# Performance work log

Hardware: AMD Instinct MI355X
Metric: run time of the kernel (lower is better)

The kernel has to match this reference:

```python
import jax, jax.numpy as jnp
import numpy as np
import math

N_HEADS = 16
D_EMBED = 1024
D_HEAD = D_EMBED // N_HEADS


def setup_inputs() -> dict:
    key = jax.random.key(0)
    ks = jax.random.split(key, 5)
    B, T = 4, 2048
    x = jax.random.normal(ks[0], (B, T, D_EMBED), dtype=jnp.float32)
    s_in = 1.0 / math.sqrt(D_EMBED)
    W_in = jax.random.normal(ks[1], (3 * D_EMBED, D_EMBED), dtype=jnp.float32) * s_in
    b_in = jax.random.normal(ks[2], (3 * D_EMBED,), dtype=jnp.float32) * s_in
    W_out = jax.random.normal(ks[3], (D_EMBED, D_EMBED), dtype=jnp.float32) * s_in
    b_out = jax.random.normal(ks[4], (D_EMBED,), dtype=jnp.float32) * s_in
    return {"x": x, "W_in": W_in, "b_in": b_in, "W_out": W_out, "b_out": b_out,
            "causal_mask": 1}


def reference(x, W_in, b_in, W_out, b_out, causal_mask):
    B, T, C = x.shape
    # in_proj: x @ W_in^T + b_in -> (B,T,3C), chunk into q,k,v
    qkv = jnp.einsum('btc,ec->bte', x, W_in) + b_in
    q, k, v = jnp.split(qkv, 3, axis=-1)
    # (B,T,H,Dh) -> (B,H,T,Dh)
    def heads(t):
        return t.reshape(B, T, N_HEADS, D_HEAD).transpose(0, 2, 1, 3)
    q, k, v = heads(q), heads(k), heads(v)
    scores = jnp.einsum('bhqd,bhkd->bhqk', q, k) / math.sqrt(D_HEAD)
    if causal_mask:
        mask = jnp.triu(jnp.ones((T, T), dtype=bool), k=1)  # True above diagonal
        scores = jnp.where(mask, -jnp.inf, scores)
    attn = jax.nn.softmax(scores, axis=-1)
    out = jnp.einsum('bhqk,bhkd->bhqd', attn, v)
    out = out.transpose(0, 2, 1, 3).reshape(B, T, C)
    out = jnp.einsum('btc,oc->bto', out, W_out) + b_out
    return out
```

## Files before the change

kernel.cpp:

```cpp
#include <hip/hip_runtime.h>
#include <hip/hip_bf16.h>

#define T_SEQ 2048
#define D_EMB 1024
#define NH    16
#define DH    64
#define NB    4
#define MROWS (NB * T_SEQ)
#define QKVN  (3 * D_EMB)

typedef __attribute__((ext_vector_type(8))) short bf16x8;
typedef __attribute__((ext_vector_type(4))) float f32x4;

__device__ __forceinline__ unsigned short f2bf(float f) {
  __hip_bfloat16 h = __float2bfloat16(f);
  return __builtin_bit_cast(unsigned short, h);
}

__device__ __forceinline__ void gload_lds16(const void* g, void* lds) {
  __builtin_amdgcn_global_load_lds(
      (const __attribute__((address_space(1))) void*)g,
      (__attribute__((address_space(3))) void*)lds, 16, 0, 0);
}

__device__ __forceinline__ float redmax16(float v) {
  v = fmaxf(v, __shfl_xor(v, 1));
  v = fmaxf(v, __shfl_xor(v, 2));
  v = fmaxf(v, __shfl_xor(v, 4));
  v = fmaxf(v, __shfl_xor(v, 8));
  return v;
}
__device__ __forceinline__ float redsum16(float v) {
  v += __shfl_xor(v, 1);
  v += __shfl_xor(v, 2);
  v += __shfl_xor(v, 4);
  v += __shfl_xor(v, 8);
  return v;
}

__global__ __launch_bounds__(256) void cvt_kernel(const float* __restrict__ in,
                                                  unsigned short* __restrict__ out,
                                                  int n4) {
  for (int i = blockIdx.x * 256 + threadIdx.x; i < n4; i += gridDim.x * 256) {
    const float4 v = reinterpret_cast<const float4*>(in)[i];
    ushort4 o;
    o.x = f2bf(v.x); o.y = f2bf(v.y); o.z = f2bf(v.z); o.w = f2bf(v.w);
    reinterpret_cast<ushort4*>(out)[i] = o;
  }
}

template <int OUT_BF16>
__global__ __launch_bounds__(256) void gemm_bt(const unsigned short* __restrict__ A,
                                               const unsigned short* __restrict__ Bt,
                                               const float* __restrict__ bias,
                                               void* __restrict__ Cout,
                                               int M, int N, int K) {
  __shared__ __align__(16) unsigned short As[128 * 32];
  __shared__ __align__(16) unsigned short Bs[128 * 32];

  const int tid = threadIdx.x;
  const int w  = tid >> 6;
  const int l  = tid & 63;
  const int lr = l & 15;
  const int lk = (l >> 4) * 8;
  const int bm = blockIdx.y * 128;
  const int bn = blockIdx.x * 128;
  const int wr = (w >> 1) * 64;
  const int wc = (w & 1) * 64;

  f32x4 acc[4][4];
#pragma unroll
  for (int i = 0; i < 4; ++i)
#pragma unroll
    for (int j = 0; j < 4; ++j) acc[i][j] = (f32x4){0.f, 0.f, 0.f, 0.f};

  const int srow = l >> 2;
  const int sk   = (l & 3) * 8;
  const unsigned short* Ab = A + (size_t)(bm + w * 32 + srow) * K + sk;
  const unsigned short* Bb = Bt + (size_t)(bn + w * 32 + srow) * K + sk;

  for (int kt = 0; kt < K; kt += 32) {
    gload_lds16(Ab + kt,                  &As[(w * 32 + 0) * 32]);
    gload_lds16(Ab + kt + (size_t)16 * K, &As[(w * 32 + 16) * 32]);
    gload_lds16(Bb + kt,                  &Bs[(w * 32 + 0) * 32]);
    gload_lds16(Bb + kt + (size_t)16 * K, &Bs[(w * 32 + 16) * 32]);
    __syncthreads();

    bf16x8 a[4], b[4];
#pragma unroll
    for (int mi = 0; mi < 4; ++mi)
      a[mi] = *reinterpret_cast<const bf16x8*>(&As[(wr + mi * 16 + lr) * 32 + lk]);
#pragma unroll
    for (int ni = 0; ni < 4; ++ni)
      b[ni] = *reinterpret_cast<const bf16x8*>(&Bs[(wc + ni * 16 + lr) * 32 + lk]);
#pragma unroll
    for (int mi = 0; mi < 4; ++mi)
#pragma unroll
      for (int ni = 0; ni < 4; ++ni)
        acc[mi][ni] = __builtin_amdgcn_mfma_f32_16x16x32_bf16(a[mi], b[ni], acc[mi][ni], 0, 0, 0);
    __syncthreads();
  }

  const int lg = l >> 4;
#pragma unroll
  for (int mi = 0; mi < 4; ++mi)
#pragma unroll
    for (int ni = 0; ni < 4; ++ni)
#pragma unroll
      for (int i = 0; i < 4; ++i) {
        const int row = bm + wr + mi * 16 + lg * 4 + i;
        const int col = bn + wc + ni * 16 + lr;
        const float v = acc[mi][ni][i] + bias[col];
        if (OUT_BF16)
          ((unsigned short*)Cout)[(size_t)row * N + col] = f2bf(v);
        else
          ((float*)Cout)[(size_t)row * N + col] = v;
      }
}

__global__ __launch_bounds__(256) void attn_fwd(const unsigned short* __restrict__ qkv,
                                                unsigned short* __restrict__ attn_out,
                                                const int* __restrict__ causal_flag) {
  __shared__ __align__(16) unsigned short Ks[64 * 64];
  __shared__ __align__(16) unsigned short Vt[64 * 64];
  __shared__ __align__(16) unsigned short Ps[4][32 * 64];

  const int tid = threadIdx.x;
  const int w  = tid >> 6;
  const int l  = tid & 63;
  const int lr = l & 15;
  const int lg = l >> 4;
  const int lk = lg * 8;
  const int bx = blockIdx.x;
  const int bh = blockIdx.y;
  const int b  = bh >> 4;
  const int h  = bh & 15;
  const int causal = causal_flag[0];

  const unsigned short* Qp = qkv + (size_t)(b * T_SEQ) * QKVN + h * DH;
  const unsigned short* Kp = Qp + D_EMB;
  const unsigned short* Vp = Qp + 2 * D_EMB;

  for (int qq = 0; qq < 2; ++qq) {
    const int qt = qq ? (15 - bx) : bx;
    const int qbase = qt * 128;

    bf16x8 qf[2][2];
#pragma unroll
    for (int mi = 0; mi < 2; ++mi)
#pragma unroll
      for (int ks = 0; ks < 2; ++ks)
        qf[mi][ks] = *reinterpret_cast<const bf16x8*>(
            Qp + (size_t)(qbase + w * 32 + mi * 16 + lr) * QKVN + ks * 32 + lk);

    f32x4 oacc[2][4];
    float mrow[2][4], lsum[2][4];
#pragma unroll
    for (int mi = 0; mi < 2; ++mi) {
#pragma unroll
      for (int di = 0; di < 4; ++di) oacc[mi][di] = (f32x4){0.f, 0.f, 0.f, 0.f};
#pragma unroll
      for (int i = 0; i < 4; ++i) { mrow[mi][i] = -INFINITY; lsum[mi][i] = 0.f; }
    }

    const int nt = causal ? (qt * 2 + 2) : (T_SEQ / 64);

    for (int kb = 0; kb < nt; ++kb) {
      const int kbase = kb * 64;
#pragma unroll
      for (int i = 0; i < 2; ++i) {
        const int rloc = w * 16 + i * 8 + (l >> 3);
        const int cj   = (l & 7) ^ (l >> 3);
        gload_lds16(Kp + (size_t)(kbase + rloc) * QKVN + cj * 8,
                    &Ks[(w * 16 + i * 8) * 64]);
      }
#pragma unroll
      for (int g2 = 0; g2 < 2; ++g2) {
        const int idx = tid + g2 * 256;
        const int k   = idx & 63;
        const int d0  = (idx >> 6) * 8;
        bf16x8 v = *reinterpret_cast<const bf16x8*>(Vp + (size_t)(kbase + k) * QKVN + d0);
#pragma unroll
        for (int j = 0; j < 8; ++j)
          Vt[(d0 + j) * 64 + (k ^ (j << 3))] = ((unsigned short*)&v)[j];
      }
      __syncthreads();

      f32x4 s[2][4];
#pragma unroll
      for (int mi = 0; mi < 2; ++mi)
#pragma unroll
        for (int ni = 0; ni < 4; ++ni) s[mi][ni] = (f32x4){0.f, 0.f, 0.f, 0.f};
#pragma unroll
      for (int ks = 0; ks < 2; ++ks) {
        bf16x8 kf[4];
#pragma unroll
        for (int ni = 0; ni < 4; ++ni) {
          const int R = ni * 16 + lr;
          kf[ni] = *reinterpret_cast<const bf16x8*>(
              &Ks[R * 64 + (((ks * 4 + lg) ^ (R & 7)) << 3)]);
        }
#pragma unroll
        for (int mi = 0; mi < 2; ++mi)
#pragma unroll
          for (int ni = 0; ni < 4; ++ni)
            s[mi][ni] = __builtin_amdgcn_mfma_f32_16x16x32_bf16(qf[mi][ks], kf[ni], s[mi][ni], 0, 0, 0);
      }

      const bool mm = causal && (kbase + 64 > qbase);
#pragma unroll
      for (int mi = 0; mi < 2; ++mi) {
#pragma unroll
        for (int i = 0; i < 4; ++i) {
          const int qrow = qbase + w * 32 + mi * 16 + lg * 4 + i;
          float rmax = -INFINITY;
#pragma unroll
          for (int ni = 0; ni < 4; ++ni) {
            float v = s[mi][ni][i] * 0.125f;
            if (mm && (kbase + ni * 16 + lr > qrow)) v = -INFINITY;
            s[mi][ni][i] = v;
            rmax = fmaxf(rmax, v);
          }
          rmax = redmax16(rmax);
          const float mnew = fmaxf(mrow[mi][i], rmax);
          const float alpha = __expf(mrow[mi][i] - mnew);
          mrow[mi][i] = mnew;
          float psum = 0.f;
#pragma unroll
          for (int ni = 0; ni < 4; ++ni) {
            const float p = __expf(s[mi][ni][i] - mnew);
            s[mi][ni][i] = p;
            psum += p;
          }
          psum = redsum16(psum);
          lsum[mi][i] = lsum[mi][i] * alpha + psum;
#pragma unroll
          for (int di = 0; di < 4; ++di) oacc[mi][di][i] *= alpha;
          const int rp = mi * 16 + lg * 4 + i;
#pragma unroll
          for (int ni = 0; ni < 4; ++ni)
            Ps[w][rp * 64 + ((ni * 16 + lr) ^ ((rp & 7) << 3))] = f2bf(s[mi][ni][i]);
        }
      }
      __syncthreads();

#pragma unroll
      for (int ks2 = 0; ks2 < 2; ++ks2) {
        bf16x8 pf[2], vf[4];
#pragma unroll
        for (int mi = 0; mi < 2; ++mi) {
          const int R = mi * 16 + lr;
          pf[mi] = *reinterpret_cast<const bf16x8*>(
              &Ps[w][R * 64 + (((ks2 * 4 + lg) ^ (R & 7)) << 3)]);
        }
#pragma unroll
        for (int di = 0; di < 4; ++di) {
          const int R = di * 16 + lr;
          vf[di] = *reinterpret_cast<const bf16x8*>(
              &Vt[R * 64 + (((ks2 * 4 + lg) ^ (R & 7)) << 3)]);
        }
#pragma unroll
        for (int mi = 0; mi < 2; ++mi)
#pragma unroll
          for (int di = 0; di < 4; ++di)
            oacc[mi][di] = __builtin_amdgcn_mfma_f32_16x16x32_bf16(pf[mi], vf[di], oacc[mi][di], 0, 0, 0);
      }
      __syncthreads();
    }

#pragma unroll
    for (int mi = 0; mi < 2; ++mi) {
#pragma unroll
      for (int i = 0; i < 4; ++i) {
        const float inv = 1.0f / lsum[mi][i];
#pragma unroll
        for (int di = 0; di < 4; ++di) {
          const int q = qbase + w * 32 + mi * 16 + lg * 4 + i;
          const int d = di * 16 + lr;
          attn_out[(size_t)(b * T_SEQ + q) * D_EMB + h * DH + d] =
              f2bf(oacc[mi][di][i] * inv);
        }
      }
    }
  }
}

extern "C" void kernel_launch(void* const* d_in, const int* in_sizes, int n_in,
                              void* d_out, int out_size, void* d_ws, size_t ws_size,
                              hipStream_t stream) {
  const float* x     = (const float*)d_in[0];
  const float* W_in  = (const float*)d_in[1];
  const float* b_in  = (const float*)d_in[2];
  const float* W_out = (const float*)d_in[3];
  const float* b_out = (const float*)d_in[4];
  const int*   causal = (const int*)d_in[5];
  float* out = (float*)d_out;

  char* ws = (char*)d_ws;
  unsigned short* x_bf    = (unsigned short*)(ws);
  unsigned short* win_bf  = (unsigned short*)(ws + 16777216);
  unsigned short* wout_bf = (unsigned short*)(ws + 23068672);
  unsigned short* qkv     = (unsigned short*)(ws + 25165824);
  unsigned short* attn    = (unsigned short*)(ws + 75497472);

  cvt_kernel<<<2048, 256, 0, stream>>>(x, x_bf, (MROWS * D_EMB) / 4);
  cvt_kernel<<<2048, 256, 0, stream>>>(W_in, win_bf, (QKVN * D_EMB) / 4);
  cvt_kernel<<<1024, 256, 0, stream>>>(W_out, wout_bf, (D_EMB * D_EMB) / 4);

  gemm_bt<1><<<dim3(QKVN / 128, MROWS / 128), 256, 0, stream>>>(
      x_bf, win_bf, b_in, qkv, MROWS, QKVN, D_EMB);

  attn_fwd<<<dim3(8, NB * NH), 256, 0, stream>>>(qkv, attn, causal);

  gemm_bt<0><<<dim3(D_EMB / 128, MROWS / 128), 256, 0, stream>>>(
      attn, wout_bf, b_out, out, MROWS, D_EMB, D_EMB);
}
```

Measured before the change: 343.0 us.

## Split attention work across 8 waves of 16 rows, skip masked tiles per wave

```diff
diff --git a/kernel.cpp b/kernel.cpp
--- a/kernel.cpp
+++ b/kernel.cpp
@@ -118,12 +118,12 @@
       }
 }
 
-__global__ __launch_bounds__(256) void attn_fwd(const unsigned short* __restrict__ qkv,
-                                                unsigned short* __restrict__ attn_out,
-                                                const int* __restrict__ causal_flag) {
+__global__ __launch_bounds__(512, 4) void attn_fwd(const unsigned short* __restrict__ qkv,
+                                                   unsigned short* __restrict__ attn_out,
+                                                   const int* __restrict__ causal_flag) {
   __shared__ __align__(16) unsigned short Ks[64 * 64];
   __shared__ __align__(16) unsigned short Vt[64 * 64];
-  __shared__ __align__(16) unsigned short Ps[4][32 * 64];
+  __shared__ __align__(16) unsigned short Ps[8][16 * 64];
 
   const int tid = threadIdx.x;
   const int w  = tid >> 6;
@@ -144,41 +144,40 @@
   for (int qq = 0; qq < 2; ++qq) {
     const int qt = qq ? (15 - bx) : bx;
     const int qbase = qt * 128;
-
-    bf16x8 qf[2][2];
-#pragma unroll
-    for (int mi = 0; mi < 2; ++mi)
-#pragma unroll
-      for (int ks = 0; ks < 2; ++ks)
-        qf[mi][ks] = *reinterpret_cast<const bf16x8*>(
-            Qp + (size_t)(qbase + w * 32 + mi * 16 + lr) * QKVN + ks * 32 + lk);
-
-    f32x4 oacc[2][4];
-    float mrow[2][4], lsum[2][4];
-#pragma unroll
-    for (int mi = 0; mi < 2; ++mi) {
-#pragma unroll
-      for (int di = 0; di < 4; ++di) oacc[mi][di] = (f32x4){0.f, 0.f, 0.f, 0.f};
-#pragma unroll
-      for (int i = 0; i < 4; ++i) { mrow[mi][i] = -INFINITY; lsum[mi][i] = 0.f; }
+    const int wrow0 = qbase + w * 16;
+
+    bf16x8 qf[2];
+#pragma unroll
+    for (int ks = 0; ks < 2; ++ks) {
+      bf16x8 v = *reinterpret_cast<const bf16x8*>(
+          Qp + (size_t)(wrow0 + lr) * QKVN + ks * 32 + lk);
+#pragma unroll
+      for (int j = 0; j < 8; ++j) {
+        const float f = __builtin_bit_cast(float, ((unsigned)(unsigned short)v[j]) << 16) * 0.125f;
+        v[j] = (short)(__builtin_bit_cast(unsigned, f) >> 16);
+      }
+      qf[ks] = v;
     }
+
+    f32x4 oacc[4];
+    float mrow[4], lsum[4];
+#pragma unroll
+    for (int di = 0; di < 4; ++di) oacc[di] = (f32x4){0.f, 0.f, 0.f, 0.f};
+#pragma unroll
+    for (int i = 0; i < 4; ++i) { mrow[i] = -INFINITY; lsum[i] = 0.f; }
 
     const int nt = causal ? (qt * 2 + 2) : (T_SEQ / 64);
 
     for (int kb = 0; kb < nt; ++kb) {
       const int kbase = kb * 64;
-#pragma unroll
-      for (int i = 0; i < 2; ++i) {
-        const int rloc = w * 16 + i * 8 + (l >> 3);
-        const int cj   = (l & 7) ^ (l >> 3);
-        gload_lds16(Kp + (size_t)(kbase + rloc) * QKVN + cj * 8,
-                    &Ks[(w * 16 + i * 8) * 64]);
-      }
-#pragma unroll
-      for (int g2 = 0; g2 < 2; ++g2) {
-        const int idx = tid + g2 * 256;
-        const int k   = idx & 63;
-        const int d0  = (idx >> 6) * 8;
+      {
+        const int cj = (l & 7) ^ (l >> 3);
+        gload_lds16(Kp + (size_t)(kbase + w * 8 + (l >> 3)) * QKVN + cj * 8,
+                    &Ks[(w * 8) * 64]);
+      }
+      {
+        const int k  = tid & 63;
+        const int d0 = (tid >> 6) * 8;
         bf16x8 v = *reinterpret_cast<const bf16x8*>(Vp + (size_t)(kbase + k) * QKVN + d0);
 #pragma unroll
         for (int j = 0; j < 8; ++j)
@@ -186,100 +185,86 @@
       }
       __syncthreads();
 
-      f32x4 s[2][4];
-#pragma unroll
-      for (int mi = 0; mi < 2; ++mi)
-#pragma unroll
-        for (int ni = 0; ni < 4; ++ni) s[mi][ni] = (f32x4){0.f, 0.f, 0.f, 0.f};
-#pragma unroll
-      for (int ks = 0; ks < 2; ++ks) {
-        bf16x8 kf[4];
-#pragma unroll
-        for (int ni = 0; ni < 4; ++ni) {
-          const int R = ni * 16 + lr;
-          kf[ni] = *reinterpret_cast<const bf16x8*>(
-              &Ks[R * 64 + (((ks * 4 + lg) ^ (R & 7)) << 3)]);
+      const bool live = !causal || (kbase <= wrow0 + 15);
+      if (live) {
+        f32x4 s[4];
+#pragma unroll
+        for (int ni = 0; ni < 4; ++ni) s[ni] = (f32x4){0.f, 0.f, 0.f, 0.f};
+#pragma unroll
+        for (int ks = 0; ks < 2; ++ks) {
+          bf16x8 kf[4];
+#pragma unroll
+          for (int ni = 0; ni < 4; ++ni) {
+            const int R = ni * 16 + lr;
+            kf[ni] = *reinterpret_cast<const bf16x8*>(
+                &Ks[R * 64 + (((ks * 4 + lg) ^ (lr & 7)) << 3)]);
+          }
+#pragma unroll
+          for (int ni = 0; ni < 4; ++ni)
+            s[ni] = __builtin_amdgcn_mfma_f32_16x16x32_bf16(qf[ks], kf[ni], s[ni], 0, 0, 0);
         }
-#pragma unroll
-        for (int mi = 0; mi < 2; ++mi)
-#pragma unroll
-          for (int ni = 0; ni < 4; ++ni)
-            s[mi][ni] = __builtin_amdgcn_mfma_f32_16x16x32_bf16(qf[mi][ks], kf[ni], s[mi][ni], 0, 0, 0);
-      }
-
-      const bool mm = causal && (kbase + 64 > qbase);
-#pragma unroll
-      for (int mi = 0; mi < 2; ++mi) {
+
+        const bool mm = causal && (kbase + 63 > wrow0);
 #pragma unroll
         for (int i = 0; i < 4; ++i) {
-          const int qrow = qbase + w * 32 + mi * 16 + lg * 4 + i;
+          const int qrow = wrow0 + lg * 4 + i;
           float rmax = -INFINITY;
 #pragma unroll
           for (int ni = 0; ni < 4; ++ni) {
-            float v = s[mi][ni][i] * 0.125f;
+            float v = s[ni][i];
             if (mm && (kbase + ni * 16 + lr > qrow)) v = -INFINITY;
-            s[mi][ni][i] = v;
+            s[ni][i] = v;
             rmax = fmaxf(rmax, v);
           }
           rmax = redmax16(rmax);
-          const float mnew = fmaxf(mrow[mi][i], rmax);
-          const float alpha = __expf(mrow[mi][i] - mnew);
-          mrow[mi][i] = mnew;
+          const float mnew = fmaxf(mrow[i], rmax);
+          const float alpha = __expf(mrow[i] - mnew);
+          mrow[i] = mnew;
           float psum = 0.f;
 #pragma unroll
           for (int ni = 0; ni < 4; ++ni) {
-            const float p = __expf(s[mi][ni][i] - mnew);
-            s[mi][ni][i] = p;
+            const float p = __expf(s[ni][i] - mnew);
+            s[ni][i] = p;
             psum += p;
           }
           psum = redsum16(psum);
-          lsum[mi][i] = lsum[mi][i] * alpha + psum;
-#pragma unroll
-          for (int di = 0; di < 4; ++di) oacc[mi][di][i] *= alpha;
-          const int rp = mi * 16 + lg * 4 + i;
+          lsum[i] = lsum[i] * alpha + psum;
+#pragma unroll
+          for (int di = 0; di < 4; ++di) oacc[di][i] *= alpha;
+          const int rp = lg * 4 + i;
 #pragma unroll
           for (int ni = 0; ni < 4; ++ni)
-            Ps[w][rp * 64 + ((ni * 16 + lr) ^ ((rp & 7) << 3))] = f2bf(s[mi][ni][i]);
+            Ps[w][rp * 64 + ((ni * 16 + lr) ^ ((rp & 7) << 3))] = f2bf(s[ni][i]);
         }
-      }
-      __syncthreads();
-
-#pragma unroll
-      for (int ks2 = 0; ks2 < 2; ++ks2) {
-        bf16x8 pf[2], vf[4];
-#pragma unroll
-        for (int mi = 0; mi < 2; ++mi) {
-          const int R = mi * 16 + lr;
-          pf[mi] = *reinterpret_cast<const bf16x8*>(
-              &Ps[w][R * 64 + (((ks2 * 4 + lg) ^ (R & 7)) << 3)]);
+
+#pragma unroll
+        for (int ks2 = 0; ks2 < 2; ++ks2) {
+          bf16x8 pf, vf[4];
+          pf = *reinterpret_cast<const bf16x8*>(
+              &Ps[w][lr * 64 + (((ks2 * 4 + lg) ^ (lr & 7)) << 3)]);
+#pragma unroll
+          for (int di = 0; di < 4; ++di) {
+            const int R = di * 16 + lr;
+            vf[di] = *reinterpret_cast<const bf16x8*>(
+                &Vt[R * 64 + (((ks2 * 4 + lg) ^ (lr & 7)) << 3)]);
+          }
+#pragma unroll
+          for (int di = 0; di < 4; ++di)
+            oacc[di] = __builtin_amdgcn_mfma_f32_16x16x32_bf16(pf, vf[di], oacc[di], 0, 0, 0);
         }
-#pragma unroll
-        for (int di = 0; di < 4; ++di) {
-          const int R = di * 16 + lr;
-          vf[di] = *reinterpret_cast<const bf16x8*>(
-              &Vt[R * 64 + (((ks2 * 4 + lg) ^ (R & 7)) << 3)]);
-        }
-#pragma unroll
-        for (int mi = 0; mi < 2; ++mi)
-#pragma unroll
-          for (int di = 0; di < 4; ++di)
-            oacc[mi][di] = __builtin_amdgcn_mfma_f32_16x16x32_bf16(pf[mi], vf[di], oacc[mi][di], 0, 0, 0);
       }
       __syncthreads();
     }
 
 #pragma unroll
-    for (int mi = 0; mi < 2; ++mi) {
-#pragma unroll
-      for (int i = 0; i < 4; ++i) {
-        const float inv = 1.0f / lsum[mi][i];
-#pragma unroll
-        for (int di = 0; di < 4; ++di) {
-          const int q = qbase + w * 32 + mi * 16 + lg * 4 + i;
-          const int d = di * 16 + lr;
-          attn_out[(size_t)(b * T_SEQ + q) * D_EMB + h * DH + d] =
-              f2bf(oacc[mi][di][i] * inv);
-        }
+    for (int i = 0; i < 4; ++i) {
+      const float inv = 1.0f / lsum[i];
+#pragma unroll
+      for (int di = 0; di < 4; ++di) {
+        const int q = wrow0 + lg * 4 + i;
+        const int d = di * 16 + lr;
+        attn_out[(size_t)(b * T_SEQ + q) * D_EMB + h * DH + d] =
+            f2bf(oacc[di][i] * inv);
       }
     }
   }
@@ -310,7 +295,7 @@
   gemm_bt<1><<<dim3(QKVN / 128, MROWS / 128), 256, 0, stream>>>(
       x_bf, win_bf, b_in, qkv, MROWS, QKVN, D_EMB);
 
-  attn_fwd<<<dim3(8, NB * NH), 256, 0, stream>>>(qkv, attn, causal);
+  attn_fwd<<<dim3(8, NB * NH), 512, 0, stream>>>(qkv, attn, causal);
 
   gemm_bt<0><<<dim3(D_EMB / 128, MROWS / 128), 256, 0, stream>>>(
       attn, wout_bf, b_out, out, MROWS, D_EMB, D_EMB);
```

Measured after the change: 322.5 us. 6.0% less time.
